# Kernel tuning notes

Hardware: AMD Instinct MI355X
Metric: run time of the kernel (lower is better)

The kernel has to match this reference:

```python
import jax, jax.numpy as jnp
import numpy as np

B = 16384       # batch size
NT = 26         # number of embedding tables
NROWS = 100000  # rows per table
M = 128         # embedding dim == bottom MLP output dim
BOT = [13, 512, 256, 128]
TOP = [479, 1024, 1024, 512, 256, 1]


def _linear_params(k, n, m):
    kw, kb = jax.random.split(k)
    W = jax.random.normal(kw, (m, n), jnp.float32) * np.sqrt(2.0 / (m + n))
    b = jax.random.normal(kb, (m,), jnp.float32) * np.sqrt(1.0 / m)
    return W, b


def setup_inputs() -> dict:
    key = jax.random.key(0)
    ks = jax.random.split(key, 16)
    dense_x = jax.random.normal(ks[0], (B, 13), jnp.float32)
    lS_i = jax.random.randint(ks[1], (NT, B), 0, NROWS, dtype=jnp.int32)
    lS_o = jnp.tile(jnp.arange(B, dtype=jnp.int32), (NT, 1))  # 1 index per bag
    s = float(np.sqrt(1.0 / NROWS))
    emb = jax.random.uniform(ks[2], (NT, NROWS, M), jnp.float32, -s, s)
    d = {"dense_x": dense_x, "lS_o": lS_o, "lS_i": lS_i, "emb": emb}
    for i in range(3):
        W, b = _linear_params(ks[3 + i], BOT[i], BOT[i + 1])
        d[f"bw{i}"] = W; d[f"bb{i}"] = b
    for i in range(5):
        W, b = _linear_params(ks[6 + i], TOP[i], TOP[i + 1])
        d[f"tw{i}"] = W; d[f"tb{i}"] = b
    return d


def _emb_bag_sum(table, idx, off):
    # nn.EmbeddingBag(mode='sum'): bag k sums rows idx[off[k]:off[k+1]]
    L = idx.shape[0]
    bag = jnp.searchsorted(off, jnp.arange(L, dtype=off.dtype), side='right') - 1
    return jax.ops.segment_sum(table[idx], bag, num_segments=B)  # [B, M]


def _forward(dense_x, emb, bws, bbs, tws, tbs, lS_o, lS_i):
    # bottom MLP (all ReLU, sigmoid_bot=-1)
    x = dense_x
    for W, b in zip(bws, bbs):
        x = jax.nn.relu(x @ W.T + b)
    # multi-table embedding-bag sum pooling
    ly = jax.vmap(_emb_bag_sum)(emb, lS_i, lS_o)          # [NT, B, M]
    # dot interaction
    T = jnp.concatenate([x[None], ly], axis=0).transpose(1, 0, 2)  # [B, NT+1, M]
    Z = jnp.einsum('bim,bjm->bij', T, T)                  # [B, 27, 27]
    li, lj = jnp.tril_indices(NT + 1, k=-1)               # pairs i>j, torch order
    Zflat = Z[:, li, lj]                                  # [B, 351]
    z = jnp.concatenate([x, Zflat], axis=1)               # [B, 479]
    # top MLP: ReLU except Sigmoid at layer index 4 (sigmoid_top=4)
    for i, (W, b) in enumerate(zip(tws, tbs)):
        z = z @ W.T + b
        z = jax.nn.sigmoid(z) if i == 4 else jax.nn.relu(z)
    return z


def reference(dense_x, lS_o, lS_i, emb,
              bw0, bb0, bw1, bb1, bw2, bb2,
              tw0, tb0, tw1, tb1, tw2, tb2, tw3, tb3, tw4, tb4):
    return _forward(dense_x, emb,
                    [bw0, bw1, bw2], [bb0, bb1, bb2],
                    [tw0, tw1, tw2, tw3, tw4], [tb0, tb1, tb2, tb3, tb4],
                    lS_o, lS_i)
```

## Files before the change

kernel.cpp:

```cpp
#include <hip/hip_runtime.h>
#include <cstdint>
#include <cstddef>

typedef _Float16 h16;
typedef __attribute__((ext_vector_type(8))) _Float16 half8;
typedef __attribute__((ext_vector_type(4))) _Float16 half4;
typedef __attribute__((ext_vector_type(2))) _Float16 half2v;
typedef __attribute__((ext_vector_type(4))) float f32x4;
typedef __attribute__((ext_vector_type(2))) float f32x2;

#define NB 16384
#define NTAB 26
#define NR 100000

__device__ __forceinline__ void gload16(const void* g, void* l) {
  __builtin_amdgcn_global_load_lds(
      (const __attribute__((address_space(1))) unsigned int*)g,
      (__attribute__((address_space(3))) unsigned int*)l, 16, 0, 0);
}

__global__ __launch_bounds__(256) void cvt_bot0_k(
    const float* __restrict__ s0, const float* __restrict__ s1,
    const float* __restrict__ s2, const float* __restrict__ s3,
    const float* __restrict__ s4, const float* __restrict__ s5,
    h16* __restrict__ dst, const float* __restrict__ x,
    const float* __restrict__ W0, const float* __restrict__ b0,
    h16* __restrict__ Y) {
  int b = blockIdx.x;
  if (b >= 9344) {
    int gid = (b - 9344) * 256 + threadIdx.x;
    int row = gid >> 9;
    int n = gid & 511;
    const float* xr = x + row * 13;
    const float* wr = W0 + n * 13;
    float acc = b0[n];
#pragma unroll
    for (int k = 0; k < 13; ++k) acc += xr[k] * wr[k];
    Y[gid] = (h16)fmaxf(acc, 0.f);
    return;
  }
  const float* src; int K, kl, i0; size_t doff;
  if (b < 512)       { src=s0; K=512;  kl=9;  i0=(b-0)*256;    doff=0; }
  else if (b < 640)  { src=s1; K=256;  kl=8;  i0=(b-512)*256;  doff=131072; }
  else if (b < 2688) { src=s2; K=479;  kl=9;  i0=(b-640)*256;  doff=163840; }
  else if (b < 6784) { src=s3; K=1024; kl=10; i0=(b-2688)*256; doff=688128; }
  else if (b < 8832) { src=s4; K=1024; kl=10; i0=(b-6784)*256; doff=1736704; }
  else               { src=s5; K=512;  kl=9;  i0=(b-8832)*256; doff=2260992; }
  int i = i0 + threadIdx.x;
  int n = i >> kl, k = i & ((1 << kl) - 1);
  dst[doff + i] = (k < K) ? (h16)src[(size_t)n * K + k] : (h16)0.f;
}

__global__ __launch_bounds__(256, 2) void mid_k(
    const h16* __restrict__ Y0, const h16* __restrict__ W1,
    const float* __restrict__ b1, const h16* __restrict__ W2,
    const float* __restrict__ b2, h16* __restrict__ Xc) {
  __shared__ __align__(16) h16 Sa[64 * 64];
  __shared__ __align__(16) h16 Sb[256 * 64];
  __shared__ __align__(16) h16 Y1[64 * 264];
  const int tid = threadIdx.x;
  const int lane = tid & 63;
  const int w = tid >> 6;
  const int l15 = lane & 15;
  const int kq = lane >> 4;
  const int l7 = lane & 7;
  const int lr8 = lane >> 3;
  const size_t row0 = (size_t)blockIdx.x * 64;

  const int sch = (lane & 7) ^ lr8;
  const h16* gA = Y0 + (row0 + w * 16 + lr8) * 512 + sch * 8;
  const h16* gB = W1 + ((size_t)w * 64 + lr8) * 512 + sch * 8;

  f32x4 acc[4][4] = {};
  for (int t = 0; t < 8; ++t) {
    const int k0 = t * 64;
#pragma unroll
    for (int i = 0; i < 2; ++i)
      gload16(gA + (size_t)i * 8 * 512 + k0, Sa + w * 1024 + i * 512);
#pragma unroll
    for (int i = 0; i < 8; ++i)
      gload16(gB + (size_t)i * 8 * 512 + k0, Sb + w * 4096 + i * 512);
    __syncthreads();
#pragma unroll
    for (int kk = 0; kk < 2; ++kk) {
      const int kb = kk * 4 + kq;
      half8 a[4], bfr[4];
#pragma unroll
      for (int mi = 0; mi < 4; ++mi)
        a[mi] = *(const half8*)&Sa[(mi * 16 + l15) * 64 + ((kb ^ l7) << 3)];
#pragma unroll
      for (int ni = 0; ni < 4; ++ni)
        bfr[ni] = *(const half8*)&Sb[(w * 64 + ni * 16 + l15) * 64 + ((kb ^ l7) << 3)];
#pragma unroll
      for (int mi = 0; mi < 4; ++mi)
#pragma unroll
        for (int ni = 0; ni < 4; ++ni)
          acc[mi][ni] = __builtin_amdgcn_mfma_f32_16x16x32_f16(bfr[ni], a[mi], acc[mi][ni], 0, 0, 0);
    }
    __syncthreads();
  }

#pragma unroll
  for (int mi = 0; mi < 4; ++mi) {
    const int row = mi * 16 + l15;
#pragma unroll
    for (int ni = 0; ni < 4; ++ni) {
      const int col = w * 64 + ni * 16 + kq * 4;
      const f32x4 bv = *(const f32x4*)&b1[col];
      half4 h;
#pragma unroll
      for (int ri = 0; ri < 4; ++ri)
        h[ri] = (h16)fmaxf(acc[mi][ni][ri] + bv[ri], 0.f);
      *(half4*)&Y1[row * 264 + col] = h;
    }
  }
  __syncthreads();

  f32x4 acc2[4][2] = {};
  for (int ks = 0; ks < 8; ++ks) {
    half8 av[4], bv[2];
#pragma unroll
    for (int mi = 0; mi < 4; ++mi)
      av[mi] = *(const half8*)&Y1[(mi * 16 + l15) * 264 + ks * 32 + kq * 8];
#pragma unroll
    for (int nf = 0; nf < 2; ++nf) {
      const int col = (w * 2 + nf) * 16 + l15;
      bv[nf] = *(const half8*)&W2[(size_t)col * 256 + ks * 32 + kq * 8];
    }
#pragma unroll
    for (int mi = 0; mi < 4; ++mi)
#pragma unroll
      for (int nf = 0; nf < 2; ++nf)
        acc2[mi][nf] = __builtin_amdgcn_mfma_f32_16x16x32_f16(bv[nf], av[mi], acc2[mi][nf], 0, 0, 0);
  }
#pragma unroll
  for (int mi = 0; mi < 4; ++mi) {
    const size_t row = row0 + mi * 16 + l15;
#pragma unroll
    for (int nf = 0; nf < 2; ++nf) {
      const int col = (w * 2 + nf) * 16 + kq * 4;
      const f32x4 bv = *(const f32x4*)&b2[col];
      half4 h;
#pragma unroll
      for (int ri = 0; ri < 4; ++ri)
        h[ri] = (h16)fmaxf(acc2[mi][nf][ri] + bv[ri], 0.f);
      *(half4*)&Xc[row * 128 + col] = h;
    }
  }
}

template <int GYL>
__global__ __launch_bounds__(256, 4) void gemm_sb(
    const h16* __restrict__ A, const h16* __restrict__ W,
    const float* __restrict__ bias, h16* __restrict__ C, int N, int K) {
  __shared__ __align__(16) h16 As[128 * 64];
  __shared__ __align__(16) h16 Bs[128 * 64];
  const int b = blockIdx.x;
  const int c8 = b & 7;
  const int q = b >> 3;
  const int jcol = q & ((1 << GYL) - 1);
  const int krow = ((q >> GYL) << 3) | c8;
  const int tid = threadIdx.x;
  const int lane = tid & 63;
  const int wave = tid >> 6;
  const int wm = wave >> 1, wn = wave & 1;
  const size_t row0 = (size_t)krow * 128;
  const size_t col0 = (size_t)jcol * 128;
  const int lr = lane >> 3;
  const int swzc = (((lane & 7) ^ lr) << 3);
  const int l15 = lane & 15;
  const int kq = lane >> 4;
  const int l7 = lane & 7;
  const int nt = K >> 6;

  const h16* ga = A + (row0 + wave * 32 + lr) * (size_t)K + swzc;
  const h16* gb = W + (col0 + wave * 32 + lr) * (size_t)K + swzc;

  f32x4 acc[4][4] = {};

  for (int t = 0; t < nt; ++t) {
    const int k0 = t << 6;
    h16* la = As + wave * 2048;
    h16* lb = Bs + wave * 2048;
#pragma unroll
    for (int i = 0; i < 4; ++i) {
      gload16(ga + (size_t)i * 8 * K + k0, la + i * 512);
      gload16(gb + (size_t)i * 8 * K + k0, lb + i * 512);
    }
    __syncthreads();
#pragma unroll
    for (int kk = 0; kk < 2; ++kk) {
      half8 a[4], bfr[4];
      const int kb = kk * 4 + kq;
#pragma unroll
      for (int mi = 0; mi < 4; ++mi)
        a[mi] = *(const half8*)&As[(wm * 64 + mi * 16 + l15) * 64 + ((kb ^ l7) << 3)];
#pragma unroll
      for (int ni = 0; ni < 4; ++ni)
        bfr[ni] = *(const half8*)&Bs[(wn * 64 + ni * 16 + l15) * 64 + ((kb ^ l7) << 3)];
#pragma unroll
      for (int mi = 0; mi < 4; ++mi)
#pragma unroll
        for (int ni = 0; ni < 4; ++ni)
          acc[mi][ni] = __builtin_amdgcn_mfma_f32_16x16x32_f16(a[mi], bfr[ni], acc[mi][ni], 0, 0, 0);
    }
    __syncthreads();
  }

#pragma unroll
  for (int mi = 0; mi < 4; ++mi)
#pragma unroll
    for (int ni = 0; ni < 4; ++ni) {
      const size_t col = col0 + wn * 64 + ni * 16 + l15;
      const float bv = bias[col];
#pragma unroll
      for (int ri = 0; ri < 4; ++ri) {
        const size_t row = row0 + wm * 64 + mi * 16 + kq * 4 + ri;
        float v = acc[mi][ni][ri] + bv;
        C[row * N + col] = (h16)fmaxf(v, 0.f);
      }
    }
}

__global__ __launch_bounds__(256, 4) void gemm_t3f(
    const h16* __restrict__ A, const h16* __restrict__ W,
    const float* __restrict__ bias, const float* __restrict__ w4,
    float* __restrict__ partial) {
  const int K = 512;
  __shared__ __align__(16) h16 As[128 * 64];
  __shared__ __align__(16) h16 Bs[128 * 64];
  const int b = blockIdx.x;
  const int c8 = b & 7;
  const int q = b >> 3;
  const int jcol = q & 1;
  const int krow = ((q >> 1) << 3) | c8;
  const int tid = threadIdx.x;
  const int lane = tid & 63;
  const int wave = tid >> 6;
  const int wm = wave >> 1, wn = wave & 1;
  const size_t row0 = (size_t)krow * 128;
  const size_t col0 = (size_t)jcol * 128;
  const int lr = lane >> 3;
  const int swzc = (((lane & 7) ^ lr) << 3);
  const int l15 = lane & 15;
  const int kq = lane >> 4;
  const int l7 = lane & 7;
  const int nt = K >> 6;

  const h16* ga = A + (row0 + wave * 32 + lr) * (size_t)K + swzc;
  const h16* gb = W + (col0 + wave * 32 + lr) * (size_t)K + swzc;

  f32x4 acc[4][4] = {};

  for (int t = 0; t < nt; ++t) {
    const int k0 = t << 6;
    h16* la = As + wave * 2048;
    h16* lb = Bs + wave * 2048;
#pragma unroll
    for (int i = 0; i < 4; ++i) {
      gload16(ga + (size_t)i * 8 * K + k0, la + i * 512);
      gload16(gb + (size_t)i * 8 * K + k0, lb + i * 512);
    }
    __syncthreads();
#pragma unroll
    for (int kk = 0; kk < 2; ++kk) {
      half8 a[4], bfr[4];
      const int kb = kk * 4 + kq;
#pragma unroll
      for (int mi = 0; mi < 4; ++mi)
        a[mi] = *(const half8*)&As[(wm * 64 + mi * 16 + l15) * 64 + ((kb ^ l7) << 3)];
#pragma unroll
      for (int ni = 0; ni < 4; ++ni)
        bfr[ni] = *(const half8*)&Bs[(wn * 64 + ni * 16 + l15) * 64 + ((kb ^ l7) << 3)];
#pragma unroll
      for (int mi = 0; mi < 4; ++mi)
#pragma unroll
        for (int ni = 0; ni < 4; ++ni)
          acc[mi][ni] = __builtin_amdgcn_mfma_f32_16x16x32_f16(a[mi], bfr[ni], acc[mi][ni], 0, 0, 0);
    }
    __syncthreads();
  }

  const int slot = jcol * 2 + wn;
#pragma unroll
  for (int mi = 0; mi < 4; ++mi) {
    float s[4] = {0.f, 0.f, 0.f, 0.f};
#pragma unroll
    for (int ni = 0; ni < 4; ++ni) {
      const size_t col = col0 + wn * 64 + ni * 16 + l15;
      const float bv = bias[col];
      const float wv = w4[col];
#pragma unroll
      for (int ri = 0; ri < 4; ++ri)
        s[ri] += fmaxf(acc[mi][ni][ri] + bv, 0.f) * wv;
    }
#pragma unroll
    for (int ri = 0; ri < 4; ++ri) {
      float v = s[ri];
      v += __shfl_xor(v, 1);
      v += __shfl_xor(v, 2);
      v += __shfl_xor(v, 4);
      v += __shfl_xor(v, 8);
      if (l15 == 0) {
        const size_t row = row0 + wm * 64 + mi * 16 + kq * 4 + ri;
        partial[(size_t)slot * NB + row] = v;
      }
    }
  }
}

__global__ __launch_bounds__(256) void sig_k(
    const float* __restrict__ partial, const float* __restrict__ bias,
    float* __restrict__ out) {
  int r = blockIdx.x * 256 + threadIdx.x;
  float v = partial[r] + partial[NB + r] + partial[2 * NB + r] +
            partial[3 * NB + r] + bias[0];
  out[r] = 1.f / (1.f + expf(-v));
}

__global__ __launch_bounds__(256) void interact_k(
    const h16* __restrict__ X, const float* __restrict__ emb,
    const int* __restrict__ lSi, h16* __restrict__ z) {
  __shared__ __align__(16) h16 T[4][32][136];
  const int lane = threadIdx.x & 63;
  const int wv = threadIdx.x >> 6;
  const size_t b = (size_t)blockIdx.x * 4 + wv;

  int idxs[NTAB];
#pragma unroll
  for (int t = 0; t < NTAB; ++t) idxs[t] = lSi[t * NB + (int)b];

  for (int i = lane; i < 5 * 128; i += 64)
    T[wv][27 + (i >> 7)][i & 127] = (h16)0.f;

  {
    half2v v = *(const half2v*)(X + b * 128 + lane * 2);
    *(half2v*)&T[wv][0][lane * 2] = v;
    *(half2v*)(z + b * 512 + lane * 2) = v;
  }
  const int thalf = lane >> 5;
  const int c4 = (lane & 31) * 4;
#pragma unroll
  for (int i = 0; i < NTAB / 2; ++i) {
    const int t = 2 * i + thalf;
    const f32x4 v = *(const f32x4*)(emb + ((size_t)t * NR + idxs[t]) * 128 + c4);
    half4 h;
#pragma unroll
    for (int j = 0; j < 4; ++j) h[j] = (h16)v[j];
    *(half4*)&T[wv][1 + t][c4] = h;
  }

  __syncthreads();

  f32x4 acc00 = {}, acc10 = {}, acc11 = {};
  const int l15 = lane & 15;
  const int kq = lane >> 4;
#pragma unroll
  for (int kk = 0; kk < 4; ++kk) {
    const int ko = kk * 32 + kq * 8;
    half8 a0 = *(const half8*)&T[wv][l15][ko];
    half8 a1 = *(const half8*)&T[wv][16 + l15][ko];
    acc00 = __builtin_amdgcn_mfma_f32_16x16x32_f16(a0, a0, acc00, 0, 0, 0);
    acc10 = __builtin_amdgcn_mfma_f32_16x16x32_f16(a1, a0, acc10, 0, 0, 0);
    acc11 = __builtin_amdgcn_mfma_f32_16x16x32_f16(a1, a1, acc11, 0, 0, 0);
  }
  h16* zr = z + b * 512 + 128;
#pragma unroll
  for (int ri = 0; ri < 4; ++ri) {
    int i0 = kq * 4 + ri;
    int i1 = 16 + i0;
    if (l15 < i0) zr[i0 * (i0 - 1) / 2 + l15] = (h16)acc00[ri];
    if (i1 < 27) {
      zr[i1 * (i1 - 1) / 2 + l15] = (h16)acc10[ri];
      int j1 = 16 + l15;
      if (j1 < i1) zr[i1 * (i1 - 1) / 2 + j1] = (h16)acc11[ri];
    }
  }
}

extern "C" void kernel_launch(void* const* d_in, const int* in_sizes, int n_in,
                              void* d_out, int out_size, void* d_ws, size_t ws_size,
                              hipStream_t stream) {
  const float* dense_x = (const float*)d_in[0];
  const int* lSi = (const int*)d_in[2];
  const float* emb = (const float*)d_in[3];
  const float* bw0 = (const float*)d_in[4];
  const float* bb0 = (const float*)d_in[5];
  const float* bw1 = (const float*)d_in[6];
  const float* bb1 = (const float*)d_in[7];
  const float* bw2 = (const float*)d_in[8];
  const float* bb2 = (const float*)d_in[9];
  const float* tw0 = (const float*)d_in[10];
  const float* tb0 = (const float*)d_in[11];
  const float* tw1 = (const float*)d_in[12];
  const float* tb1 = (const float*)d_in[13];
  const float* tw2 = (const float*)d_in[14];
  const float* tb2 = (const float*)d_in[15];
  const float* tw3 = (const float*)d_in[16];
  const float* tb3 = (const float*)d_in[17];
  const float* tw4 = (const float*)d_in[18];
  const float* tb4 = (const float*)d_in[19];
  float* out = (float*)d_out;

  char* ws = (char*)d_ws;
  const size_t MB = (size_t)1 << 20;
  h16* Y0 = (h16*)(ws + 0 * MB);
  h16* Xc = (h16*)(ws + 24 * MB);
  h16* Zz = (h16*)(ws + 32 * MB);
  h16* U0 = (h16*)(ws + 48 * MB);
  h16* U1 = (h16*)(ws + 0 * MB);
  h16* U2 = (h16*)(ws + 32 * MB);
  float* partial = (float*)(ws + 48 * MB);
  h16* w1p = (h16*)(ws + 80 * MB);
  h16* w2p = w1p + 256 * 512;
  h16* t0p = w2p + 128 * 256;
  h16* t1p = t0p + 1024 * 512;
  h16* t2p = t1p + 1024 * 1024;
  h16* t3p = t2p + 512 * 1024;
  (void)in_sizes; (void)n_in; (void)out_size; (void)ws_size;

  cvt_bot0_k<<<9344 + 32768, 256, 0, stream>>>(bw1, bw2, tw0, tw1, tw2, tw3,
                                               w1p, dense_x, bw0, bb0, Y0);
  mid_k<<<256, 256, 0, stream>>>(Y0, w1p, bb1, w2p, bb2, Xc);
  interact_k<<<NB / 4, 256, 0, stream>>>(Xc, emb, lSi, Zz);
  gemm_sb<3><<<128 * 8, 256, 0, stream>>>(Zz, t0p, tb0, U0, 1024, 512);
  gemm_sb<3><<<128 * 8, 256, 0, stream>>>(U0, t1p, tb1, U1, 1024, 1024);
  gemm_sb<2><<<128 * 4, 256, 0, stream>>>(U1, t2p, tb2, U2, 512, 1024);
  gemm_t3f<<<128 * 2, 256, 0, stream>>>(U2, t3p, tb3, tw4, partial);
  sig_k<<<NB / 256, 256, 0, stream>>>(partial, tb4, out);
}
```

Baseline: 205.7 us.

## Widen top-MLP GEMM tiles to 256x128 per block

```diff
diff --git a/kernel.cpp b/kernel.cpp
--- a/kernel.cpp
+++ b/kernel.cpp
@@ -150,10 +150,10 @@
 }
 
 template <int GYL>
-__global__ __launch_bounds__(256, 4) void gemm_sb(
+__global__ __launch_bounds__(256, 2) void gemm_wd(
     const h16* __restrict__ A, const h16* __restrict__ W,
     const float* __restrict__ bias, h16* __restrict__ C, int N, int K) {
-  __shared__ __align__(16) h16 As[128 * 64];
+  __shared__ __align__(16) h16 As[256 * 64];
   __shared__ __align__(16) h16 Bs[128 * 64];
   const int b = blockIdx.x;
   const int c8 = b & 7;
@@ -164,58 +164,57 @@
   const int lane = tid & 63;
   const int wave = tid >> 6;
   const int wm = wave >> 1, wn = wave & 1;
-  const size_t row0 = (size_t)krow * 128;
+  const size_t row0 = (size_t)krow * 256;
   const size_t col0 = (size_t)jcol * 128;
-  const int lr = lane >> 3;
-  const int swzc = (((lane & 7) ^ lr) << 3);
   const int l15 = lane & 15;
   const int kq = lane >> 4;
   const int l7 = lane & 7;
   const int nt = K >> 6;
 
-  const h16* ga = A + (row0 + wave * 32 + lr) * (size_t)K + swzc;
-  const h16* gb = W + (col0 + wave * 32 + lr) * (size_t)K + swzc;
-
-  f32x4 acc[4][4] = {};
+  const int srow = tid >> 3;
+  const int swc = ((tid & 7) ^ (srow & 7)) << 3;
+  const h16* ga = A + (row0 + srow) * (size_t)K + swc;
+  const h16* gb = W + (col0 + srow) * (size_t)K + swc;
+
+  f32x4 acc[8][4] = {};
 
   for (int t = 0; t < nt; ++t) {
     const int k0 = t << 6;
-    h16* la = As + wave * 2048;
-    h16* lb = Bs + wave * 2048;
-#pragma unroll
-    for (int i = 0; i < 4; ++i) {
-      gload16(ga + (size_t)i * 8 * K + k0, la + i * 512);
-      gload16(gb + (size_t)i * 8 * K + k0, lb + i * 512);
-    }
+#pragma unroll
+    for (int i = 0; i < 8; ++i)
+      gload16(ga + (size_t)(i * 32) * K + k0, As + i * 2048 + tid * 8);
+#pragma unroll
+    for (int i = 0; i < 4; ++i)
+      gload16(gb + (size_t)(i * 32) * K + k0, Bs + i * 2048 + tid * 8);
     __syncthreads();
 #pragma unroll
     for (int kk = 0; kk < 2; ++kk) {
-      half8 a[4], bfr[4];
       const int kb = kk * 4 + kq;
-#pragma unroll
-      for (int mi = 0; mi < 4; ++mi)
-        a[mi] = *(const half8*)&As[(wm * 64 + mi * 16 + l15) * 64 + ((kb ^ l7) << 3)];
+      const int sl = (kb ^ l7) << 3;
+      half8 bfr[4];
 #pragma unroll
       for (int ni = 0; ni < 4; ++ni)
-        bfr[ni] = *(const half8*)&Bs[(wn * 64 + ni * 16 + l15) * 64 + ((kb ^ l7) << 3)];
-#pragma unroll
-      for (int mi = 0; mi < 4; ++mi)
+        bfr[ni] = *(const half8*)&Bs[(wn * 64 + ni * 16 + l15) * 64 + sl];
+#pragma unroll
+      for (int mi = 0; mi < 8; ++mi) {
+        half8 av = *(const half8*)&As[(wm * 128 + mi * 16 + l15) * 64 + sl];
 #pragma unroll
         for (int ni = 0; ni < 4; ++ni)
-          acc[mi][ni] = __builtin_amdgcn_mfma_f32_16x16x32_f16(a[mi], bfr[ni], acc[mi][ni], 0, 0, 0);
-    }
-    __syncthreads();
-  }
-
-#pragma unroll
-  for (int mi = 0; mi < 4; ++mi)
+          acc[mi][ni] = __builtin_amdgcn_mfma_f32_16x16x32_f16(av, bfr[ni], acc[mi][ni], 0, 0, 0);
+      }
+    }
+    __syncthreads();
+  }
+
+#pragma unroll
+  for (int mi = 0; mi < 8; ++mi)
 #pragma unroll
     for (int ni = 0; ni < 4; ++ni) {
       const size_t col = col0 + wn * 64 + ni * 16 + l15;
       const float bv = bias[col];
 #pragma unroll
       for (int ri = 0; ri < 4; ++ri) {
-        const size_t row = row0 + wm * 64 + mi * 16 + kq * 4 + ri;
+        const size_t row = row0 + wm * 128 + mi * 16 + kq * 4 + ri;
         float v = acc[mi][ni][ri] + bv;
         C[row * N + col] = (h16)fmaxf(v, 0.f);
       }
@@ -423,9 +422,9 @@
                                                w1p, dense_x, bw0, bb0, Y0);
   mid_k<<<256, 256, 0, stream>>>(Y0, w1p, bb1, w2p, bb2, Xc);
   interact_k<<<NB / 4, 256, 0, stream>>>(Xc, emb, lSi, Zz);
-  gemm_sb<3><<<128 * 8, 256, 0, stream>>>(Zz, t0p, tb0, U0, 1024, 512);
-  gemm_sb<3><<<128 * 8, 256, 0, stream>>>(U0, t1p, tb1, U1, 1024, 1024);
-  gemm_sb<2><<<128 * 4, 256, 0, stream>>>(U1, t2p, tb2, U2, 512, 1024);
+  gemm_wd<3><<<64 * 8, 256, 0, stream>>>(Zz, t0p, tb0, U0, 1024, 512);
+  gemm_wd<3><<<64 * 8, 256, 0, stream>>>(U0, t1p, tb1, U1, 1024, 1024);
+  gemm_wd<2><<<64 * 4, 256, 0, stream>>>(U1, t2p, tb2, U2, 512, 1024);
   gemm_t3f<<<128 * 2, 256, 0, stream>>>(U2, t3p, tb3, tw4, partial);
   sig_k<<<NB / 256, 256, 0, stream>>>(partial, tb4, out);
 }
```

After: 206.9 us. About the same (+0.6%).
